# Kernel optimization log

Measured on AMD Instinct MI355X. Metric: run time of the kernel, lower is better.

The kernel has to match this reference:

```python
import jax, jax.numpy as jnp
import numpy as np

H = 768  # bert-base hidden size; match MLP width = 2*H = 1536


def setup_inputs() -> dict:
    key = jax.random.key(0)
    ks = jax.random.split(key, 6)
    B, S = 2, 256
    std = 0.02  # TruncatedNormal(stddev=initializer_range)
    return {
        "hidden": jax.random.normal(ks[0], (B, S, H), dtype=jnp.float32),
        "w_start": jax.random.normal(ks[1], (H, 1), dtype=jnp.float32) * std,
        "b_start": jnp.zeros((1,), jnp.float32),
        "w_end": jax.random.normal(ks[2], (H, 1), dtype=jnp.float32) * std,
        "b_end": jnp.zeros((1,), jnp.float32),
        "w1": jax.random.normal(ks[3], (2 * H, 2 * H), dtype=jnp.float32) * std,
        "b1": jnp.zeros((2 * H,), jnp.float32),
        "w2": jax.random.normal(ks[4], (2 * H, 1), dtype=jnp.float32) * std,
        "b2": jnp.zeros((1,), jnp.float32),
    }


def reference(hidden, w_start, b_start, w_end, b_end, w1, b1, w2, b2):
    # hidden: [B, S, H] = BERT sequence output (dropout disabled at inference)
    start_logits = hidden @ w_start + b_start  # [B, S, 1]
    end_logits = hidden @ w_end + b_end        # [B, S, 1]

    # Pairwise span features: concat(row_i, col_j) along last dim, fed to dense1.
    # concat([row, col]) @ w1 == row @ w1[:H] + col @ w1[H:], so we split w1 and
    # broadcast-add instead of materializing the [B,S,S,2H] concat tile.
    row_proj = hidden @ w1[:H]   # [B, S, 2H] (start-token contribution)
    col_proj = hidden @ w1[H:]   # [B, S, 2H] (end-token contribution)
    pre = row_proj[:, :, None, :] + col_proj[:, None, :, :] + b1  # [B, S, S, 2H]
    act = jax.nn.gelu(pre, approximate=False)  # keras 'gelu' is exact
    match_logits = act @ w2 + b2  # [B, S, S, 1]
    return start_logits, end_logits, match_logits
```

## Files before the change

kernel.cpp:

```cpp
#include <hip/hip_runtime.h>
#include <stdint.h>

typedef __attribute__((ext_vector_type(8))) __bf16 bf16x8;
typedef __attribute__((ext_vector_type(4))) float  floatx4;
typedef __attribute__((ext_vector_type(4))) unsigned int uint4v;
typedef __attribute__((ext_vector_type(2))) unsigned int uint2v;
typedef __attribute__((ext_vector_type(4))) float  float4v;
typedef __attribute__((ext_vector_type(2))) _Float16 half2v;

__device__ __forceinline__ unsigned short f2bf(float f) {
  union { float f; unsigned int u; } x; x.f = f;
  unsigned int r = x.u + 0x7fffu + ((x.u >> 16) & 1u);
  return (unsigned short)(r >> 16);
}

__global__ __launch_bounds__(256) void proj_kernel(
    const float* __restrict__ hidden, const float* __restrict__ w1,
    const float* __restrict__ b1, unsigned short* __restrict__ wsR,
    unsigned short* __restrict__ wsC,
    const float* __restrict__ w_start, const float* __restrict__ b_start,
    const float* __restrict__ w_end, const float* __restrict__ b_end,
    const float* __restrict__ b2, float* __restrict__ out) {
  const int tid  = threadIdx.x;
  if (blockIdx.y == 16) {
    if (blockIdx.x >= 32) {
      float v = b2[0];
      float4v vv = {v, v, v, v};
      int base = (blockIdx.x - 32) * 8192 + tid * 4;
#pragma unroll
      for (int itr = 0; itr < 8; ++itr)
        *(float4v*)(out + 1024 + base + itr * 1024) = vv;
      return;
    }
    const int lane = tid & 63;
    const int wv   = tid >> 6;
    const int wg   = blockIdx.x * 4 + wv;
    float wsv[12], wev[12];
#pragma unroll
    for (int t = 0; t < 12; ++t) {
      wsv[t] = w_start[lane + 64 * t];
      wev[t] = w_end[lane + 64 * t];
    }
    const float bs = b_start[0];
    const float be = b_end[0];
#pragma unroll
    for (int r = 0; r < 4; ++r) {
      int row = wg * 4 + r;
      const float* h = hidden + (size_t)row * 768;
      float ps = 0.f, pe = 0.f;
#pragma unroll
      for (int t = 0; t < 12; ++t) {
        float hv = h[lane + 64 * t];
        ps += hv * wsv[t];
        pe += hv * wev[t];
      }
#pragma unroll
      for (int off = 32; off >= 1; off >>= 1) {
        ps += __shfl_xor(ps, off, 64);
        pe += __shfl_xor(pe, off, 64);
      }
      if (lane == 0) { out[row] = ps + bs; out[512 + row] = pe + be; }
    }
    return;
  }

  __shared__ short As[4 * 32 * 8];
  __shared__ short Bs[4 * 64 * 8];

  const int lane = tid & 63;
  const int wave = tid >> 6;
  const int wr = wave >> 1, wc = wave & 1;
  const int m0 = blockIdx.y * 32;
  const int n0g = blockIdx.x * 64;
  const bool isR = (n0g < 1536);
  const int kbase = isR ? 0 : 768;
  const int n0 = isR ? n0g : (n0g - 1536);
  const int q = lane >> 4, l15 = lane & 15;

  floatx4 acc0 = {}, acc1 = {};

  const int a_row = tid >> 3;
  const int a_s   = tid & 7;
  const int b_n   = tid & 63;
  const int b_kg  = tid >> 6;

  const float* hrow = hidden + (size_t)(m0 + a_row) * 768 + a_s * 4;
  const float* bcol = w1 + (size_t)(kbase + b_kg * 8) * 1536 + n0 + b_n;

  float4v hv = *(const float4v*)(hrow);
  float bv[8];
#pragma unroll
  for (int a = 0; a < 8; ++a) bv[a] = bcol[(size_t)a * 1536];

  const int aq = a_s >> 1;
  const int aj = (a_s & 1) * 4;

  for (int ko = 0; ko < 768; ko += 32) {
    uint2v au;
    au[0] = (unsigned int)f2bf(hv[0]) | ((unsigned int)f2bf(hv[1]) << 16);
    au[1] = (unsigned int)f2bf(hv[2]) | ((unsigned int)f2bf(hv[3]) << 16);
    *(uint2v*)(&As[(aq * 32 + a_row) * 8 + aj]) = au;
    uint4v pv;
#pragma unroll
    for (int a = 0; a < 4; ++a) {
      unsigned int lo = f2bf(bv[2 * a]);
      unsigned int hi = f2bf(bv[2 * a + 1]);
      pv[a] = lo | (hi << 16);
    }
    *(uint4v*)(&Bs[(b_kg * 64 + b_n) * 8]) = pv;
    __syncthreads();

    if (ko + 32 < 768) {
      hv = *(const float4v*)(hrow + ko + 32);
      const float* bp = bcol + (size_t)(ko + 32) * 1536;
#pragma unroll
      for (int a = 0; a < 8; ++a) bv[a] = bp[(size_t)a * 1536];
    }

    bf16x8 af  = *(const bf16x8*)(&As[(q * 32 + 16 * wr + l15) * 8]);
    bf16x8 bg0 = *(const bf16x8*)(&Bs[(q * 64 + 32 * wc + l15) * 8]);
    bf16x8 bg1 = *(const bf16x8*)(&Bs[(q * 64 + 32 * wc + 16 + l15) * 8]);
    acc0 = __builtin_amdgcn_mfma_f32_16x16x32_bf16(af, bg0, acc0, 0, 0, 0);
    acc1 = __builtin_amdgcn_mfma_f32_16x16x32_bf16(af, bg1, acc1, 0, 0, 0);
    __syncthreads();
  }

  unsigned short* outp = isR ? wsR : wsC;
#pragma unroll
  for (int ni = 0; ni < 2; ++ni) {
    const floatx4& ac = ni ? acc1 : acc0;
    int col = n0 + 32 * wc + 16 * ni + l15;
    float bias = isR ? b1[col] : 0.0f;
#pragma unroll
    for (int r = 0; r < 4; ++r) {
      int rowg = m0 + 16 * wr + q * 4 + r;
      outp[(size_t)rowg * 1536 + col] = f2bf(ac[r] + bias);
    }
  }
}

__device__ __forceinline__ void gelu_pair(float& acc, unsigned int ru,
                                          unsigned int cu, unsigned int wu) {
  const half2v C3 = {(_Float16)-1.51033e-4f, (_Float16)-1.51033e-4f};
  const half2v C2 = {(_Float16)0.00461682f, (_Float16)0.00461682f};
  const half2v C1 = {(_Float16)-0.05415410f, (_Float16)-0.05415410f};
  const half2v C0 = {(_Float16)0.39103831f, (_Float16)0.39103831f};
  const half2v HI = {(_Float16)3.5f, (_Float16)3.5f};
  const half2v LO = {(_Float16)-3.5f, (_Float16)-3.5f};
  const half2v HALF = {(_Float16)0.5f, (_Float16)0.5f};
  half2v r = __builtin_bit_cast(half2v, ru);
  half2v c = __builtin_bit_cast(half2v, cu);
  half2v w = __builtin_bit_cast(half2v, wu);
  half2v x = r + c;
  half2v xc = __builtin_elementwise_min(
      __builtin_elementwise_max(x, LO), HI);
  half2v u = xc * xc;
  half2v p = __builtin_elementwise_fma(u,
      __builtin_elementwise_fma(u,
          __builtin_elementwise_fma(u, C3, C2), C1), C0);
  half2v t = __builtin_elementwise_fma(xc, p, HALF);
  half2v g = x * t;
  acc = __builtin_amdgcn_fdot2(g, w, acc, false);
}

__device__ __forceinline__ uint4v bf8_to_h8(uint4v v) {
  uint4v o;
#pragma unroll
  for (int a = 0; a < 4; ++a) {
    union { unsigned int u; float f; } lo, hi;
    lo.u = v[a] << 16;
    hi.u = v[a] & 0xffff0000u;
    auto h = __builtin_amdgcn_cvt_pkrtz(lo.f, hi.f);
    o[a] = __builtin_bit_cast(unsigned int, h);
  }
  return o;
}

__global__ __launch_bounds__(256) void match_kernel(
    const unsigned short* __restrict__ wsR,
    const unsigned short* __restrict__ wsC,
    const float* __restrict__ w2,
    float* __restrict__ outm) {
  __shared__ unsigned int RsU[32 * 36];
  __shared__ unsigned int CsU[64 * 36];
  __shared__ unsigned int WsU[32];

  const int tid = threadIdx.x;
  const int jt = blockIdx.x;
  const int it = blockIdx.y;
  const int bz = blockIdx.z / 24;
  const int kh = blockIdx.z % 24;
  const int Kb = kh * 64;

  const int rg  = tid >> 4;
  const int cgl = tid & 15;

  float accA0 = 0.f, accA1 = 0.f, accA2 = 0.f, accA3 = 0.f;
  float accB0 = 0.f, accB1 = 0.f, accB2 = 0.f, accB3 = 0.f;

  const int srow = tid >> 3;
  const int sseg = tid & 7;
  {
    const unsigned short* g =
        wsR + (size_t)(bz * 256 + it * 32 + srow) * 1536 + Kb + sseg * 8;
    *(uint4v*)(RsU + srow * 36 + sseg * 4) = bf8_to_h8(*(const uint4v*)g);
  }
#pragma unroll
  for (int a = 0; a < 2; ++a) {
    int row = srow + 32 * a;
    const unsigned short* g =
        wsC + (size_t)(bz * 256 + jt * 64 + row) * 1536 + Kb + sseg * 8;
    *(uint4v*)(CsU + row * 36 + sseg * 4) = bf8_to_h8(*(const uint4v*)g);
  }
  if (tid < 32) {
    auto h = __builtin_amdgcn_cvt_pkrtz(w2[Kb + 2 * tid], w2[Kb + 2 * tid + 1]);
    WsU[tid] = __builtin_bit_cast(unsigned int, h);
  }
  __syncthreads();

  const unsigned int* rap = RsU + (2 * rg + 0) * 36;
  const unsigned int* rbp = RsU + (2 * rg + 1) * 36;
  const unsigned int* c0p = CsU + (cgl +  0) * 36;
  const unsigned int* c1p = CsU + (cgl + 16) * 36;
  const unsigned int* c2p = CsU + (cgl + 32) * 36;
  const unsigned int* c3p = CsU + (cgl + 48) * 36;

#pragma unroll 2
  for (int ks = 0; ks < 8; ++ks) {
    uint4v ra = *(const uint4v*)(rap + ks * 4);
    uint4v rb = *(const uint4v*)(rbp + ks * 4);
    uint4v wv = *(const uint4v*)(WsU + ks * 4);
    {
      uint4v cv = *(const uint4v*)(c0p + ks * 4);
#pragma unroll
      for (int p = 0; p < 4; ++p) {
        gelu_pair(accA0, ra[p], cv[p], wv[p]);
        gelu_pair(accB0, rb[p], cv[p], wv[p]);
      }
    }
    {
      uint4v cv = *(const uint4v*)(c1p + ks * 4);
#pragma unroll
      for (int p = 0; p < 4; ++p) {
        gelu_pair(accA1, ra[p], cv[p], wv[p]);
        gelu_pair(accB1, rb[p], cv[p], wv[p]);
      }
    }
    {
      uint4v cv = *(const uint4v*)(c2p + ks * 4);
#pragma unroll
      for (int p = 0; p < 4; ++p) {
        gelu_pair(accA2, ra[p], cv[p], wv[p]);
        gelu_pair(accB2, rb[p], cv[p], wv[p]);
      }
    }
    {
      uint4v cv = *(const uint4v*)(c3p + ks * 4);
#pragma unroll
      for (int p = 0; p < 4; ++p) {
        gelu_pair(accA3, ra[p], cv[p], wv[p]);
        gelu_pair(accB3, rb[p], cv[p], wv[p]);
      }
    }
  }

  const size_t rowA = (size_t)(bz * 256 + it * 32 + 2 * rg);
  const size_t base = rowA * 256 + jt * 64 + cgl;
  unsafeAtomicAdd(&outm[base +  0], accA0);
  unsafeAtomicAdd(&outm[base + 16], accA1);
  unsafeAtomicAdd(&outm[base + 32], accA2);
  unsafeAtomicAdd(&outm[base + 48], accA3);
  unsafeAtomicAdd(&outm[base + 256 +  0], accB0);
  unsafeAtomicAdd(&outm[base + 256 + 16], accB1);
  unsafeAtomicAdd(&outm[base + 256 + 32], accB2);
  unsafeAtomicAdd(&outm[base + 256 + 48], accB3);
}

extern "C" void kernel_launch(void* const* d_in, const int* in_sizes, int n_in,
                              void* d_out, int out_size, void* d_ws, size_t ws_size,
                              hipStream_t stream) {
  const float* hidden  = (const float*)d_in[0];
  const float* w_start = (const float*)d_in[1];
  const float* b_start = (const float*)d_in[2];
  const float* w_end   = (const float*)d_in[3];
  const float* b_end   = (const float*)d_in[4];
  const float* w1      = (const float*)d_in[5];
  const float* b1      = (const float*)d_in[6];
  const float* w2      = (const float*)d_in[7];
  const float* b2      = (const float*)d_in[8];

  float* out = (float*)d_out;
  char* ws = (char*)d_ws;
  unsigned short* wsR = (unsigned short*)(ws);
  unsigned short* wsC = (unsigned short*)(ws + 1572864);

  proj_kernel<<<dim3(48, 17), dim3(256), 0, stream>>>(
      hidden, w1, b1, wsR, wsC, w_start, b_start, w_end, b_end, b2, out);
  match_kernel<<<dim3(4, 8, 48), dim3(256), 0, stream>>>(wsR, wsC, w2, out + 1024);
}
```

Before: 123.6 us.

## Pre-convert inputs to bf16, use inline packed-f16 asm, double match K-chunk

Adds a separate conversion kernel that writes hidden and w1 to bf16 in workspace, so the projection GEMM loads half the bytes and skips per-iteration float-to-bf16 rounding. The GELU helper is rewritten with inline v_pk_*_f16 asm and hoisted packed constants. The match kernel's K chunk per block doubles from 64 to 128, which halves the number of blocks and atomic adds. The cost is an extra kernel launch plus a full pass over w1, fewer blocks in the match grid, and inline asm that may limit compiler scheduling.

```diff
diff --git a/kernel.cpp b/kernel.cpp
--- a/kernel.cpp
+++ b/kernel.cpp
@@ -7,6 +7,7 @@
 typedef __attribute__((ext_vector_type(2))) unsigned int uint2v;
 typedef __attribute__((ext_vector_type(4))) float  float4v;
 typedef __attribute__((ext_vector_type(2))) _Float16 half2v;
+typedef unsigned int u32;
 
 __device__ __forceinline__ unsigned short f2bf(float f) {
   union { float f; unsigned int u; } x; x.f = f;
@@ -14,8 +15,26 @@
   return (unsigned short)(r >> 16);
 }
 
+__global__ __launch_bounds__(256) void convert_kernel(
+    const float* __restrict__ hidden, const float* __restrict__ w1,
+    unsigned short* __restrict__ wsH, unsigned short* __restrict__ wsW1) {
+  int t = blockIdx.x * 256 + threadIdx.x;
+  const float* src; unsigned short* dst; int idx;
+  if (t < 49152) { src = hidden; dst = wsH; idx = t * 8; }
+  else           { src = w1;     dst = wsW1; idx = (t - 49152) * 8; }
+  float4v v0 = *(const float4v*)(src + idx);
+  float4v v1 = *(const float4v*)(src + idx + 4);
+  uint4v o;
+  o[0] = (u32)f2bf(v0[0]) | ((u32)f2bf(v0[1]) << 16);
+  o[1] = (u32)f2bf(v0[2]) | ((u32)f2bf(v0[3]) << 16);
+  o[2] = (u32)f2bf(v1[0]) | ((u32)f2bf(v1[1]) << 16);
+  o[3] = (u32)f2bf(v1[2]) | ((u32)f2bf(v1[3]) << 16);
+  *(uint4v*)(dst + idx) = o;
+}
+
 __global__ __launch_bounds__(256) void proj_kernel(
-    const float* __restrict__ hidden, const float* __restrict__ w1,
+    const unsigned short* __restrict__ wsH, const unsigned short* __restrict__ wsW1,
+    const float* __restrict__ hidden,
     const float* __restrict__ b1, unsigned short* __restrict__ wsR,
     unsigned short* __restrict__ wsC,
     const float* __restrict__ w_start, const float* __restrict__ b_start,
@@ -84,11 +103,11 @@
   const int b_n   = tid & 63;
   const int b_kg  = tid >> 6;
 
-  const float* hrow = hidden + (size_t)(m0 + a_row) * 768 + a_s * 4;
-  const float* bcol = w1 + (size_t)(kbase + b_kg * 8) * 1536 + n0 + b_n;
-
-  float4v hv = *(const float4v*)(hrow);
-  float bv[8];
+  const unsigned short* hrow = wsH + (size_t)(m0 + a_row) * 768 + a_s * 4;
+  const unsigned short* bcol = wsW1 + (size_t)(kbase + b_kg * 8) * 1536 + n0 + b_n;
+
+  uint2v au = *(const uint2v*)(hrow);
+  unsigned short bv[8];
 #pragma unroll
   for (int a = 0; a < 8; ++a) bv[a] = bcol[(size_t)a * 1536];
 
@@ -96,23 +115,17 @@
   const int aj = (a_s & 1) * 4;
 
   for (int ko = 0; ko < 768; ko += 32) {
-    uint2v au;
-    au[0] = (unsigned int)f2bf(hv[0]) | ((unsigned int)f2bf(hv[1]) << 16);
-    au[1] = (unsigned int)f2bf(hv[2]) | ((unsigned int)f2bf(hv[3]) << 16);
     *(uint2v*)(&As[(aq * 32 + a_row) * 8 + aj]) = au;
     uint4v pv;
 #pragma unroll
-    for (int a = 0; a < 4; ++a) {
-      unsigned int lo = f2bf(bv[2 * a]);
-      unsigned int hi = f2bf(bv[2 * a + 1]);
-      pv[a] = lo | (hi << 16);
-    }
+    for (int a = 0; a < 4; ++a)
+      pv[a] = (u32)bv[2 * a] | ((u32)bv[2 * a + 1] << 16);
     *(uint4v*)(&Bs[(b_kg * 64 + b_n) * 8]) = pv;
     __syncthreads();
 
     if (ko + 32 < 768) {
-      hv = *(const float4v*)(hrow + ko + 32);
-      const float* bp = bcol + (size_t)(ko + 32) * 1536;
+      au = *(const uint2v*)(hrow + ko + 32);
+      const unsigned short* bp = bcol + (size_t)(ko + 32) * 1536;
 #pragma unroll
       for (int a = 0; a < 8; ++a) bv[a] = bp[(size_t)a * 1536];
     }
@@ -139,28 +152,38 @@
   }
 }
 
-__device__ __forceinline__ void gelu_pair(float& acc, unsigned int ru,
-                                          unsigned int cu, unsigned int wu) {
-  const half2v C3 = {(_Float16)-1.51033e-4f, (_Float16)-1.51033e-4f};
-  const half2v C2 = {(_Float16)0.00461682f, (_Float16)0.00461682f};
-  const half2v C1 = {(_Float16)-0.05415410f, (_Float16)-0.05415410f};
-  const half2v C0 = {(_Float16)0.39103831f, (_Float16)0.39103831f};
-  const half2v HI = {(_Float16)3.5f, (_Float16)3.5f};
-  const half2v LO = {(_Float16)-3.5f, (_Float16)-3.5f};
-  const half2v HALF = {(_Float16)0.5f, (_Float16)0.5f};
-  half2v r = __builtin_bit_cast(half2v, ru);
-  half2v c = __builtin_bit_cast(half2v, cu);
-  half2v w = __builtin_bit_cast(half2v, wu);
-  half2v x = r + c;
-  half2v xc = __builtin_elementwise_min(
-      __builtin_elementwise_max(x, LO), HI);
-  half2v u = xc * xc;
-  half2v p = __builtin_elementwise_fma(u,
-      __builtin_elementwise_fma(u,
-          __builtin_elementwise_fma(u, C3, C2), C1), C0);
-  half2v t = __builtin_elementwise_fma(xc, p, HALF);
-  half2v g = x * t;
-  acc = __builtin_amdgcn_fdot2(g, w, acc, false);
+__device__ __forceinline__ u32 ph_add(u32 a, u32 b) {
+  u32 d; asm("v_pk_add_f16 %0, %1, %2" : "=v"(d) : "v"(a), "v"(b)); return d;
+}
+__device__ __forceinline__ u32 ph_mul(u32 a, u32 b) {
+  u32 d; asm("v_pk_mul_f16 %0, %1, %2" : "=v"(d) : "v"(a), "v"(b)); return d;
+}
+__device__ __forceinline__ u32 ph_fma(u32 a, u32 b, u32 c) {
+  u32 d; asm("v_pk_fma_f16 %0, %1, %2, %3" : "=v"(d) : "v"(a), "v"(b), "v"(c)); return d;
+}
+__device__ __forceinline__ u32 ph_max(u32 a, u32 b) {
+  u32 d; asm("v_pk_max_f16 %0, %1, %2" : "=v"(d) : "v"(a), "v"(b)); return d;
+}
+__device__ __forceinline__ u32 ph_min(u32 a, u32 b) {
+  u32 d; asm("v_pk_min_f16 %0, %1, %2" : "=v"(d) : "v"(a), "v"(b)); return d;
+}
+__device__ __forceinline__ u32 h2c(float f) {
+  _Float16 h = (_Float16)f;
+  unsigned short s = __builtin_bit_cast(unsigned short, h);
+  return (u32)s | ((u32)s << 16);
+}
+
+__device__ __forceinline__ void gelu_pair(float& acc, u32 r, u32 c, u32 w,
+                                          u32 C0c, u32 C1c, u32 C2c, u32 C3c,
+                                          u32 LOc, u32 HIc, u32 Hc) {
+  u32 x  = ph_add(r, c);
+  u32 xc = ph_min(ph_max(x, LOc), HIc);
+  u32 u  = ph_mul(xc, xc);
+  u32 p  = ph_fma(u, ph_fma(u, ph_fma(u, C3c, C2c), C1c), C0c);
+  u32 t  = ph_fma(xc, p, Hc);
+  u32 g  = ph_mul(x, t);
+  acc = __builtin_amdgcn_fdot2(__builtin_bit_cast(half2v, g),
+                               __builtin_bit_cast(half2v, w), acc, false);
 }
 
 __device__ __forceinline__ uint4v bf8_to_h8(uint4v v) {
@@ -181,52 +204,64 @@
     const unsigned short* __restrict__ wsC,
     const float* __restrict__ w2,
     float* __restrict__ outm) {
-  __shared__ unsigned int RsU[32 * 36];
-  __shared__ unsigned int CsU[64 * 36];
-  __shared__ unsigned int WsU[32];
+  __shared__ unsigned int RsU[32 * 68];
+  __shared__ unsigned int CsU[64 * 68];
+  __shared__ unsigned int WsU[64];
 
   const int tid = threadIdx.x;
   const int jt = blockIdx.x;
   const int it = blockIdx.y;
-  const int bz = blockIdx.z / 24;
-  const int kh = blockIdx.z % 24;
-  const int Kb = kh * 64;
+  const int bz = blockIdx.z / 12;
+  const int kh = blockIdx.z % 12;
+  const int Kb = kh * 128;
 
   const int rg  = tid >> 4;
   const int cgl = tid & 15;
 
+  const u32 C0c = h2c(0.39103831f);
+  const u32 C1c = h2c(-0.05415410f);
+  const u32 C2c = h2c(0.00461682f);
+  const u32 C3c = h2c(-1.51033e-4f);
+  const u32 LOc = h2c(-3.5f);
+  const u32 HIc = h2c(3.5f);
+  const u32 Hc  = h2c(0.5f);
+
   float accA0 = 0.f, accA1 = 0.f, accA2 = 0.f, accA3 = 0.f;
   float accB0 = 0.f, accB1 = 0.f, accB2 = 0.f, accB3 = 0.f;
 
   const int srow = tid >> 3;
   const int sseg = tid & 7;
-  {
+#pragma unroll
+  for (int ps = 0; ps < 2; ++ps) {
     const unsigned short* g =
-        wsR + (size_t)(bz * 256 + it * 32 + srow) * 1536 + Kb + sseg * 8;
-    *(uint4v*)(RsU + srow * 36 + sseg * 4) = bf8_to_h8(*(const uint4v*)g);
+        wsR + (size_t)(bz * 256 + it * 32 + srow) * 1536 + Kb + ps * 64 + sseg * 8;
+    *(uint4v*)(RsU + srow * 68 + ps * 32 + sseg * 4) = bf8_to_h8(*(const uint4v*)g);
   }
 #pragma unroll
   for (int a = 0; a < 2; ++a) {
     int row = srow + 32 * a;
-    const unsigned short* g =
-        wsC + (size_t)(bz * 256 + jt * 64 + row) * 1536 + Kb + sseg * 8;
-    *(uint4v*)(CsU + row * 36 + sseg * 4) = bf8_to_h8(*(const uint4v*)g);
-  }
-  if (tid < 32) {
+#pragma unroll
+    for (int ps = 0; ps < 2; ++ps) {
+      const unsigned short* g =
+          wsC + (size_t)(bz * 256 + jt * 64 + row) * 1536 + Kb + ps * 64 + sseg * 8;
+      *(uint4v*)(CsU + row * 68 + ps * 32 + sseg * 4) = bf8_to_h8(*(const uint4v*)g);
+    }
+  }
+  if (tid < 64) {
     auto h = __builtin_amdgcn_cvt_pkrtz(w2[Kb + 2 * tid], w2[Kb + 2 * tid + 1]);
     WsU[tid] = __builtin_bit_cast(unsigned int, h);
   }
   __syncthreads();
 
-  const unsigned int* rap = RsU + (2 * rg + 0) * 36;
-  const unsigned int* rbp = RsU + (2 * rg + 1) * 36;
-  const unsigned int* c0p = CsU + (cgl +  0) * 36;
-  const unsigned int* c1p = CsU + (cgl + 16) * 36;
-  const unsigned int* c2p = CsU + (cgl + 32) * 36;
-  const unsigned int* c3p = CsU + (cgl + 48) * 36;
+  const unsigned int* rap = RsU + (2 * rg + 0) * 68;
+  const unsigned int* rbp = RsU + (2 * rg + 1) * 68;
+  const unsigned int* c0p = CsU + (cgl +  0) * 68;
+  const unsigned int* c1p = CsU + (cgl + 16) * 68;
+  const unsigned int* c2p = CsU + (cgl + 32) * 68;
+  const unsigned int* c3p = CsU + (cgl + 48) * 68;
 
 #pragma unroll 2
-  for (int ks = 0; ks < 8; ++ks) {
+  for (int ks = 0; ks < 16; ++ks) {
     uint4v ra = *(const uint4v*)(rap + ks * 4);
     uint4v rb = *(const uint4v*)(rbp + ks * 4);
     uint4v wv = *(const uint4v*)(WsU + ks * 4);
@@ -234,32 +269,32 @@
       uint4v cv = *(const uint4v*)(c0p + ks * 4);
 #pragma unroll
       for (int p = 0; p < 4; ++p) {
-        gelu_pair(accA0, ra[p], cv[p], wv[p]);
-        gelu_pair(accB0, rb[p], cv[p], wv[p]);
+        gelu_pair(accA0, ra[p], cv[p], wv[p], C0c, C1c, C2c, C3c, LOc, HIc, Hc);
+        gelu_pair(accB0, rb[p], cv[p], wv[p], C0c, C1c, C2c, C3c, LOc, HIc, Hc);
       }
     }
     {
       uint4v cv = *(const uint4v*)(c1p + ks * 4);
 #pragma unroll
       for (int p = 0; p < 4; ++p) {
-        gelu_pair(accA1, ra[p], cv[p], wv[p]);
-        gelu_pair(accB1, rb[p], cv[p], wv[p]);
+        gelu_pair(accA1, ra[p], cv[p], wv[p], C0c, C1c, C2c, C3c, LOc, HIc, Hc);
+        gelu_pair(accB1, rb[p], cv[p], wv[p], C0c, C1c, C2c, C3c, LOc, HIc, Hc);
       }
     }
     {
       uint4v cv = *(const uint4v*)(c2p + ks * 4);
 #pragma unroll
       for (int p = 0; p < 4; ++p) {
-        gelu_pair(accA2, ra[p], cv[p], wv[p]);
-        gelu_pair(accB2, rb[p], cv[p], wv[p]);
+        gelu_pair(accA2, ra[p], cv[p], wv[p], C0c, C1c, C2c, C3c, LOc, HIc, Hc);
+        gelu_pair(accB2, rb[p], cv[p], wv[p], C0c, C1c, C2c, C3c, LOc, HIc, Hc);
       }
     }
     {
       uint4v cv = *(const uint4v*)(c3p + ks * 4);
 #pragma unroll
       for (int p = 0; p < 4; ++p) {
-        gelu_pair(accA3, ra[p], cv[p], wv[p]);
-        gelu_pair(accB3, rb[p], cv[p], wv[p]);
+        gelu_pair(accA3, ra[p], cv[p], wv[p], C0c, C1c, C2c, C3c, LOc, HIc, Hc);
+        gelu_pair(accB3, rb[p], cv[p], wv[p], C0c, C1c, C2c, C3c, LOc, HIc, Hc);
       }
     }
   }
@@ -291,10 +326,13 @@
 
   float* out = (float*)d_out;
   char* ws = (char*)d_ws;
-  unsigned short* wsR = (unsigned short*)(ws);
-  unsigned short* wsC = (unsigned short*)(ws + 1572864);
-
+  unsigned short* wsR  = (unsigned short*)(ws);
+  unsigned short* wsC  = (unsigned short*)(ws + 1572864);
+  unsigned short* wsH  = (unsigned short*)(ws + 3145728);
+  unsigned short* wsW1 = (unsigned short*)(ws + 3932160);
+
+  convert_kernel<<<dim3(1344), dim3(256), 0, stream>>>(hidden, w1, wsH, wsW1);
   proj_kernel<<<dim3(48, 17), dim3(256), 0, stream>>>(
-      hidden, w1, b1, wsR, wsC, w_start, b_start, w_end, b_end, b2, out);
-  match_kernel<<<dim3(4, 8, 48), dim3(256), 0, stream>>>(wsR, wsC, w2, out + 1024);
-}
+      wsH, wsW1, hidden, b1, wsR, wsC, w_start, b_start, w_end, b_end, b2, out);
+  match_kernel<<<dim3(4, 8, 24), dim3(256), 0, stream>>>(wsR, wsC, w2, out + 1024);
+}
```

Result: slower. 129.0 us (+4.3%).
